# Kernel optimization log

Measured on AMD Instinct MI355X. Metric: run time of the kernel, lower is better.

## Reference

```python
import jax, jax.numpy as jnp
import numpy as np

NPG = 39      # nodes per graph, from (1+8+64+9)*(39+1)=3280 = lin1 in_features
NEG_SLOPE = 0.2


def gat_conv(x, src, dst, W, a_src, a_dst, b, n):
    """PyG GATConv, heads=1, self-loops already appended to (src, dst).
    x:[N,Fin] W:[Fin,Fout] a_src/a_dst:[Fout] b:[Fout] -> [N,Fout]"""
    h = x @ W                                        # [N,Fout]
    e = jax.nn.leaky_relu(h[src] @ a_src + h[dst] @ a_dst, NEG_SLOPE)  # [E]
    m = jax.lax.stop_gradient(jax.ops.segment_max(e, dst, num_segments=n))
    w = jnp.exp(e - m[dst])
    denom = jax.ops.segment_sum(w, dst, num_segments=n)
    alpha = w / (denom[dst] + 1e-16)                 # segment softmax per target node
    out = jax.ops.segment_sum(alpha[:, None] * h[src], dst, num_segments=n)
    return out + b


def setup_inputs() -> dict:
    key = jax.random.key(0)
    ks = jax.random.split(key, 20)
    B, DEG = 4096, 8
    N = B * NPG
    E = N * DEG
    x = jax.random.normal(ks[0], (N, 1), dtype=jnp.float32)
    # block-diagonal edges: each node emits DEG edges to random nodes in SAME graph
    src = jnp.repeat(jnp.arange(N, dtype=jnp.int64), DEG)
    offs = (src // NPG) * NPG
    dst = offs + jax.random.randint(ks[1], (E,), 0, NPG, dtype=jnp.int64)
    edge_index = jnp.stack([src, dst])
    batch_vec = jnp.repeat(jnp.arange(B, dtype=jnp.int64), NPG)

    def glorot(k, shape):
        fan = shape[0] + (shape[1] if len(shape) > 1 else 1)
        s = jnp.sqrt(6.0 / fan)
        return jax.random.uniform(k, shape, jnp.float32, -s, s)

    p = {
        'W1': glorot(ks[2], (1, 8)),   'a1s': glorot(ks[3], (8,)),  'a1d': glorot(ks[4], (8,)),  'b1': jnp.zeros((8,), jnp.float32),
        'W2': glorot(ks[5], (8, 64)),  'a2s': glorot(ks[6], (64,)), 'a2d': glorot(ks[7], (64,)), 'b2': jnp.zeros((64,), jnp.float32),
        'W3': glorot(ks[8], (64, 9)),  'a3s': glorot(ks[9], (9,)),  'a3d': glorot(ks[10], (9,)), 'b3': jnp.zeros((9,), jnp.float32),
        'lW1': glorot(ks[11], (3280, 5000)), 'lb1': jnp.zeros((5000,), jnp.float32),
        'lW2': glorot(ks[12], (5000, 1024)), 'lb2': jnp.zeros((1024,), jnp.float32),
        'lW3': glorot(ks[13], (1024, 9)),    'lb3': jnp.zeros((9,), jnp.float32),
    }
    return {'x': x, 'edge_index': edge_index, 'batch_vec': batch_vec, **p}


def reference(x, edge_index, batch_vec,
              W1, a1s, a1d, b1, W2, a2s, a2d, b2, W3, a3s, a3d, b3,
              lW1, lb1, lW2, lb2, lW3, lb3):
    N = x.shape[0]
    B = N // NPG
    loops = jnp.arange(N, dtype=edge_index.dtype)
    src = jnp.concatenate([edge_index[0], loops])   # GATConv add_self_loops=True
    dst = jnp.concatenate([edge_index[1], loops])

    res = x.reshape(B, -1)                                    # [B,39]
    out0 = jax.ops.segment_max(x, batch_vec, num_segments=B)  # [B,1]

    h1 = jax.nn.relu(gat_conv(x, src, dst, W1, a1s, a1d, b1, N))   # dropout = eval no-op
    res1 = h1.reshape(B, -1)                                   # [B,312]
    out1 = jax.ops.segment_max(h1, batch_vec, num_segments=B)

    h2 = jax.nn.relu(gat_conv(h1, src, dst, W2, a2s, a2d, b2, N))
    res2 = h2.reshape(B, -1)                                   # [B,2496]
    out2 = jax.ops.segment_max(h2, batch_vec, num_segments=B)

    h3 = jax.nn.relu(gat_conv(h2, src, dst, W3, a3s, a3d, b3, N))
    res3 = h3.reshape(B, -1)                                   # [B,351]
    out3 = jax.ops.segment_max(h3, batch_vec, num_segments=B)

    f = jnp.concatenate([res, res1, res2, res3, out0, out1, out2, out3], axis=1)  # [B,3280]
    f = jax.nn.relu(f @ lW1 + lb1)
    f = jax.nn.relu(f @ lW2 + lb2)
    return f @ lW3 + lb3                                       # [B,9]
```

## Files before the change

kernel.cpp:

```cpp
#include <hip/hip_runtime.h>
#include <hip/hip_bf16.h>
#include <hip/hip_fp16.h>
#include <stdint.h>


typedef float f32x4 __attribute__((ext_vector_type(4)));
typedef short bf16x8 __attribute__((ext_vector_type(8)));


__device__ __forceinline__ void seg_softmax(
    float* al, const unsigned short* sl, const int* off, float* sa,
    const float* dbuf, int L)
{
  if (L < 39) {
    int p0 = off[L], p1 = off[L + 1];
    float d = dbuf[L];
    float mx = -1e30f;
    for (int p = p0; p < p1; ++p) {
      float e = sa[sl[p]] + d;
      e = (e > 0.f) ? e : 0.2f * e;
      al[p] = e; mx = fmaxf(mx, e);
    }
    float den = 0.f;
    for (int p = p0; p < p1; ++p) { float wv = __expf(al[p] - mx); al[p] = wv; den += wv; }
    sa[L] = 1.f / (den + 1e-16f);
  }
}

__global__ __launch_bounds__(128) void gnn_block(
    const float* __restrict__ x,
    const int* __restrict__ esrc, const int* __restrict__ edst,
    const float* __restrict__ W1, const float* __restrict__ a1s, const float* __restrict__ a1d, const float* __restrict__ b1,
    const float* __restrict__ W2, const float* __restrict__ a2s, const float* __restrict__ a2d, const float* __restrict__ b2,
    const float* __restrict__ W3, const float* __restrict__ a3s, const float* __restrict__ a3d, const float* __restrict__ b3,
    __hip_bfloat16* __restrict__ fA)
{
  __shared__ __align__(16) char HtU[5152];
  __shared__ __align__(16) __half h2buf[2576];
  __shared__ float h3b[352];
  __shared__ __half h1h[320];
  __shared__ float al[352];
  __shared__ unsigned short sl[352];
  __shared__ int off[40];
  __shared__ int cur[40];
  __shared__ float sa[40], dbuf[40], xbuf[40];
  __shared__ float a2buf[128];
  __shared__ float mx[132];
  __shared__ float sW3s[576];

  const int tid = threadIdx.x, g = blockIdx.x;
  float* Hf  = (float*)HtU;
  __half* Hh = (__half*)HtU;

  const int rt = g >> 7, mi = (g >> 4) & 7, lrow = g & 15;
  const size_t gbase = (size_t)rt * 52 * 8192 + (size_t)(mi * 2) * 512 + (size_t)lrow * 8;
#define COLADDR(c) (gbase + (size_t)((c) >> 6) * 8192 + (size_t)(((c) >> 5) & 1) * 512 \
                    + (size_t)(((c) >> 3) & 3) * 128 + ((c) & 7))

  for (int i = tid; i < 576; i += 128) sW3s[i] = W3[i];
  a2buf[tid] = (tid < 64) ? a2s[tid] : a2d[tid - 64];
  float xv = 0.f;
  if (tid < 40) cur[tid] = 0;
  if (tid < 39) { xv = x[g * 39 + tid]; xbuf[tid] = xv; }

  if (tid < 64) {
    float m = (tid < 39) ? xv : -1e30f;
    for (int o = 32; o >= 1; o >>= 1) m = fmaxf(m, __shfl_xor(m, o, 64));
    if (tid == 0) mx[0] = m;
  }
  if (tid < 39) fA[COLADDR(tid)] = __float2bfloat16(xv);
  __syncthreads();

  int els[3], eld[3];
  const int eb = g * 312, nb0 = g * 39;
#pragma unroll
  for (int it = 0; it < 3; ++it) {
    int e = it * 128 + tid, ls = -1, ld = 0;
    if (e < 351) {
      if (e < 312) { ls = esrc[eb + e] - nb0; ld = edst[eb + e] - nb0; }
      else         { ls = e - 312; ld = ls; }
      atomicAdd(&cur[ld], 1);
    }
    els[it] = ls; eld[it] = ld;
  }
  __syncthreads();
  if (tid < 64) {
    int c = (tid < 39) ? cur[tid] : 0;
    int incl = c;
    for (int o = 1; o < 64; o <<= 1) { int t = __shfl_up(incl, o, 64); if (tid >= o) incl += t; }
    if (tid < 39) off[tid] = incl - c;
    if (tid == 38) off[39] = incl;
  }
  __syncthreads();
  if (tid < 39) cur[tid] = off[tid];
  __syncthreads();
#pragma unroll
  for (int it = 0; it < 3; ++it)
    if (els[it] >= 0) { int p = atomicAdd(&cur[eld[it]], 1); sl[p] = (unsigned short)els[it]; }
  __syncthreads();

  {
    const float w1r = W1[tid & 7];
#pragma unroll
    for (int it = 0; it < 3; ++it) {
      int slot = it * 128 + tid;
      if (slot < 312) { int i = slot >> 3, fi = slot & 7; Hf[i * 9 + fi] = xbuf[i] * w1r; }
    }
  }
  __syncthreads();
  {
    int node = tid & 63;
    if (node < 39) {
      const float* av = (tid < 64) ? a1s : a1d;
      float s = 0.f;
#pragma unroll
      for (int f = 0; f < 8; ++f) s += Hf[node * 9 + f] * av[f];
      if (tid < 64) sa[node] = s; else dbuf[node] = s;
    }
  }
  __syncthreads();
  if (tid < 64) seg_softmax(al, sl, off, sa, dbuf, tid);
  __syncthreads();
  {
    const float b1r = b1[tid & 7];
#pragma unroll
    for (int it = 0; it < 3; ++it) {
      int slot = it * 128 + tid;
      if (slot < 312) {
        int i = slot >> 3, fi = slot & 7;
        float acc = 0.f;
        int p1 = off[i + 1];
        for (int p = off[i]; p < p1; ++p) acc += al[p] * Hf[sl[p] * 9 + fi];
        float v = fmaxf(acc * sa[i] + b1r, 0.f);
        h1h[i * 8 + fi] = __float2half(v);
        int c = 39 + slot;
        fA[COLADDR(c)] = __float2bfloat16(v);
      }
    }
  }
  __syncthreads();

  {
    const int f = tid & 63;
    float w2k[8];
#pragma unroll
    for (int k = 0; k < 8; ++k) w2k[k] = W2[k * 64 + f];
    for (int it = 0; it < 20; ++it) {
      int i = it * 2 + (tid >> 6);
      if (i < 39) {
        float hv = 0.f;
#pragma unroll
        for (int k = 0; k < 8; ++k) hv += __half2float(h1h[i * 8 + k]) * w2k[k];
        Hh[i * 66 + f] = __float2half(hv);
      }
    }
  }
  __syncthreads();
  {
    int node = tid & 63;
    if (node < 39) {
      const float* ab = a2buf + (tid & 64);
      float s = 0.f;
      for (int f = 0; f < 64; ++f) s += __half2float(Hh[node * 66 + f]) * ab[f];
      if (tid < 64) sa[node] = s; else dbuf[node] = s;
    }
  }
  __syncthreads();
  if (tid < 64) seg_softmax(al, sl, off, sa, dbuf, tid);
  __syncthreads();
  {
    const int f = tid & 63;
    const float b2r = b2[f];
    for (int it = 0; it < 20; ++it) {
      int i = it * 2 + (tid >> 6);
      if (i < 39) {
        float acc = 0.f;
        int p1 = off[i + 1];
        for (int p = off[i]; p < p1; ++p) acc += al[p] * __half2float(Hh[sl[p] * 66 + f]);
        float v = fmaxf(acc * sa[i] + b2r, 0.f);
        h2buf[i * 66 + f] = __float2half(v);
        int c = 351 + i * 64 + f;
        fA[COLADDR(c)] = __float2bfloat16(v);
      }
    }
  }
  __syncthreads();

  {
#pragma unroll
    for (int it = 0; it < 3; ++it) {
      int slot = it * 128 + tid;
      if (slot < 351) {
        int i = slot / 9, f3 = slot - 9 * i;
        float acc = 0.f;
        for (int k = 0; k < 64; ++k) acc += __half2float(h2buf[i * 66 + k]) * sW3s[k * 9 + f3];
        Hf[i * 10 + f3] = acc;
      }
    }
  }
  __syncthreads();
  {
    int node = tid & 63;
    if (node < 39) {
      const float* av = (tid < 64) ? a3s : a3d;
      float s = 0.f;
#pragma unroll
      for (int f3 = 0; f3 < 9; ++f3) s += Hf[node * 10 + f3] * av[f3];
      if (tid < 64) sa[node] = s; else dbuf[node] = s;
    }
  }
  __syncthreads();
  if (tid < 64) seg_softmax(al, sl, off, sa, dbuf, tid);
  __syncthreads();
  {
#pragma unroll
    for (int it = 0; it < 3; ++it) {
      int slot = it * 128 + tid;
      if (slot < 351) {
        int i = slot / 9, f3 = slot - 9 * i;
        float acc = 0.f;
        int p1 = off[i + 1];
        for (int p = off[i]; p < p1; ++p) acc += al[p] * Hf[sl[p] * 10 + f3];
        float v = fmaxf(acc * sa[i] + b3[f3], 0.f);
        h3b[slot] = v;
        int c = 2847 + slot;
        fA[COLADDR(c)] = __float2bfloat16(v);
      }
    }
  }
  __syncthreads();

  if (tid >= 1 && tid < 9) {
    int f = tid - 1; float m = -1e30f;
    for (int i = 0; i < 39; ++i) m = fmaxf(m, __half2float(h1h[i * 8 + f]));
    mx[tid] = m;
  } else if (tid >= 9 && tid < 73) {
    int f = tid - 9; float m = -1e30f;
    for (int i = 0; i < 39; ++i) m = fmaxf(m, __half2float(h2buf[i * 66 + f]));
    mx[tid] = m;
  } else if (tid >= 73 && tid < 82) {
    int f = tid - 73; float m = -1e30f;
    for (int i = 0; i < 39; ++i) m = fmaxf(m, h3b[i * 9 + f]);
    mx[tid] = m;
  } else if (tid >= 82 && tid < 130) {
    mx[tid] = 0.f;
  }
  __syncthreads();
  if (tid < 130) {
    int c = 3198 + tid;
    fA[COLADDR(c)] = __float2bfloat16(mx[tid]);
  }
#undef COLADDR
}


__global__ __launch_bounds__(256) void conv_tiled(
    const float* __restrict__ W, short* __restrict__ WT,
    int K0, int N0, int KT)
{
  __shared__ float t[64][68];
  const int kb = blockIdx.x * 64, nb = blockIdx.y * 64;
  const int tid = threadIdx.x;
  const int tx = tid & 15, ty = tid >> 4;
#pragma unroll
  for (int r = 0; r < 4; ++r) {
    int k = kb + ty + r * 16, n = nb + tx * 4;
    float4 v = make_float4(0.f, 0.f, 0.f, 0.f);
    if (k < K0 && n < N0) v = *(const float4*)&W[(size_t)k * N0 + n];
    t[ty + r * 16][tx * 4 + 0] = v.x; t[ty + r * 16][tx * 4 + 1] = v.y;
    t[ty + r * 16][tx * 4 + 2] = v.z; t[ty + r * 16][tx * 4 + 3] = v.w;
  }
  __syncthreads();
  const int nl = tid >> 2, kc0 = tid & 3;
#pragma unroll
  for (int h = 0; h < 2; ++h) {
    int kc = kc0 + h * 4;
    int n = nb + nl, k = kb + kc * 8;
    union { bf16x8 v; __hip_bfloat16 b[8]; } z;
#pragma unroll
    for (int j = 0; j < 8; ++j) z.b[j] = __float2bfloat16(t[kc * 8 + j][nl]);
    int rt = n >> 7, mi = (n >> 4) & 7, lr = n & 15;
    int kt = k >> 6, kq = (k >> 5) & 1, lc = (k >> 3) & 3;
    size_t addr = ((((size_t)rt * KT) + kt) * 16 + mi * 2 + kq) * 512 + ((size_t)lr + 16 * lc) * 8;
    *(bf16x8*)&WT[addr] = z.v;
  }
}


__device__ __forceinline__ void gld_lds16(const void* gptr, void* l) {
  typedef const __attribute__((address_space(1))) unsigned int GU;
  typedef __attribute__((address_space(3))) unsigned int LU;
  __builtin_amdgcn_global_load_lds((GU*)gptr, (LU*)l, 16, 0, 0);
}

template<int MODE>
__global__ __launch_bounds__(256) void gemm_tiled(
    const short* __restrict__ A, const short* __restrict__ B,
    const float* __restrict__ bias, int Nreal,
    void* __restrict__ Cout, int Nn, int KT, int ktPerSplit, int outKT)
{
  __shared__ __align__(16) short lA[8192];
  __shared__ __align__(16) short lB[8192];
  const int tid = threadIdx.x;
  const int w = tid >> 6, L = tid & 63;
  const int lrow = L & 15, lch = L >> 4;
  const int mt = blockIdx.y, nt = blockIdx.x;
  const int mw = (w >> 1) * 4, nw = (w & 1) * 4;
  const int kt0 = blockIdx.z * ktPerSplit, kt1 = kt0 + ktPerSplit;

  const short* Ab = A + ((size_t)mt * KT) * 8192 + (size_t)L * 8;
  const short* Bb = B + ((size_t)nt * KT) * 8192 + (size_t)L * 8;

  f32x4 acc[4][4] = {};

  for (int kt = kt0; kt < kt1; ++kt) {
    const short* Ak = Ab + (size_t)kt * 8192;
    const short* Bk = Bb + (size_t)kt * 8192;
#pragma unroll
    for (int j = 0; j < 4; ++j) {
      int st = w * 4 + j;
      gld_lds16(Ak + st * 512, &lA[st * 512]);
      gld_lds16(Bk + st * 512, &lB[st * 512]);
    }
    __syncthreads();
#pragma unroll
    for (int kk = 0; kk < 2; ++kk) {
      bf16x8 af[4], bfr[4];
#pragma unroll
      for (int i = 0; i < 4; ++i) {
        af[i]  = *(const bf16x8*)&lA[((mw + i) * 2 + kk) * 512 + L * 8];
        bfr[i] = *(const bf16x8*)&lB[((nw + i) * 2 + kk) * 512 + L * 8];
      }
#pragma unroll
      for (int i = 0; i < 4; ++i)
#pragma unroll
        for (int j = 0; j < 4; ++j)
          acc[i][j] = __builtin_amdgcn_mfma_f32_16x16x32_bf16(af[i], bfr[j], acc[i][j], 0, 0, 0);
    }
    __syncthreads();
  }

  if (MODE == 0) {
    __hip_bfloat16* C = (__hip_bfloat16*)Cout;
#pragma unroll
    for (int j = 0; j < 4; ++j) {
      int n = nt * 128 + (nw + j) * 16 + lrow;
      float bn = (n < Nreal) ? bias[n] : 0.f;
      int kt = n >> 6, kq = (n >> 5) & 1, lc2 = (n >> 3) & 3, j2 = n & 7;
#pragma unroll
      for (int i = 0; i < 4; ++i) {
        int mi = mw + i;
        size_t base = ((((size_t)mt * outKT + kt) * 16) + mi * 2 + kq) * 512
                      + (size_t)(lch * 4) * 8 + (size_t)lc2 * 128 + j2;
#pragma unroll
        for (int r = 0; r < 4; ++r)
          C[base + r * 8] = __float2bfloat16(fmaxf(acc[i][j][r] + bn, 0.f));
      }
    }
  } else {
    float* P = (float*)Cout + (size_t)blockIdx.z * 4096 * 1024;
#pragma unroll
    for (int j = 0; j < 4; ++j) {
      int n = nt * 128 + (nw + j) * 16 + lrow;
#pragma unroll
      for (int i = 0; i < 4; ++i)
#pragma unroll
        for (int r = 0; r < 4; ++r) {
          int m = mt * 128 + (mw + i) * 16 + lch * 4 + r;
          P[(size_t)m * Nn + n] = acc[i][j][r];
        }
    }
  }
}


__global__ __launch_bounds__(256) void gemm3_fused(
    const float* __restrict__ P,
    const float* __restrict__ b2v,
    const float* __restrict__ W3,
    const float* __restrict__ b3v,
    float* __restrict__ out)
{
  __shared__ float sW3[9 * 1024];
  int tid = threadIdx.x;
  for (int i = tid; i < 9216; i += 256) { int k = i / 9, j = i - 9 * k; sW3[j * 1024 + k] = W3[i]; }
  __syncthreads();
  int row = blockIdx.x * 4 + (tid >> 6);
  int lane = tid & 63;
  const float* p0 = P + (size_t)row * 1024;
  const float* p1 = p0 + (size_t)4096 * 1024;
  float acc[9] = {0, 0, 0, 0, 0, 0, 0, 0, 0};
  for (int t = 0; t < 16; ++t) {
    int k = lane + 64 * t;
    float c = fmaxf(p0[k] + p1[k] + b2v[k], 0.f);
#pragma unroll
    for (int j = 0; j < 9; ++j) acc[j] += c * sW3[j * 1024 + k];
  }
#pragma unroll
  for (int j = 0; j < 9; ++j) {
    float v = acc[j];
    v += __shfl_down(v, 32, 64);
    v += __shfl_down(v, 16, 64);
    v += __shfl_down(v, 8, 64);
    v += __shfl_down(v, 4, 64);
    v += __shfl_down(v, 2, 64);
    v += __shfl_down(v, 1, 64);
    if (lane == 0) out[(size_t)row * 9 + j] = v + b3v[j];
  }
}


extern "C" void kernel_launch(void* const* d_in, const int* in_sizes, int n_in,
                              void* d_out, int out_size, void* d_ws, size_t ws_size,
                              hipStream_t stream)
{
  const float* x   = (const float*)d_in[0];
  const int*   ei  = (const int*)d_in[1];
  const float* W1  = (const float*)d_in[3];
  const float* a1s = (const float*)d_in[4];
  const float* a1d = (const float*)d_in[5];
  const float* b1  = (const float*)d_in[6];
  const float* W2  = (const float*)d_in[7];
  const float* a2s = (const float*)d_in[8];
  const float* a2d = (const float*)d_in[9];
  const float* b2  = (const float*)d_in[10];
  const float* W3  = (const float*)d_in[11];
  const float* a3s = (const float*)d_in[12];
  const float* a3d = (const float*)d_in[13];
  const float* b3  = (const float*)d_in[14];
  const float* lW1 = (const float*)d_in[15];
  const float* lb1 = (const float*)d_in[16];
  const float* lW2 = (const float*)d_in[17];
  const float* lb2 = (const float*)d_in[18];
  const float* lW3 = (const float*)d_in[19];
  const float* lb3 = (const float*)d_in[20];

  const int E = 4096 * 39 * 8;
  const int* esrc = ei;
  const int* edst = ei + E;

  short* fA  = (short*)d_ws;
  short* W1T = fA  + (size_t)4096 * 3328;
  short* C1  = W1T + (size_t)5120 * 3328;
  short* W2T = C1  + (size_t)4096 * 5120;
  float* P   = (float*)d_ws;

  conv_tiled<<<dim3(3328 / 64, 5120 / 64), 256, 0, stream>>>(lW1, W1T, 3280, 5000, 52);
  conv_tiled<<<dim3(5120 / 64, 1024 / 64), 256, 0, stream>>>(lW2, W2T, 5000, 1024, 80);
  gnn_block<<<4096, 128, 0, stream>>>(x, esrc, edst,
                                      W1, a1s, a1d, b1, W2, a2s, a2d, b2, W3, a3s, a3d, b3,
                                      (__hip_bfloat16*)fA);
  gemm_tiled<0><<<dim3(40, 32, 1), 256, 0, stream>>>(fA, W1T, lb1, 5000, C1, 5120, 52, 52, 80);
  gemm_tiled<1><<<dim3(8, 32, 2), 256, 0, stream>>>(C1, W2T, nullptr, 1024, P, 1024, 80, 40, 0);
  gemm3_fused<<<1024, 256, 0, stream>>>(P, lb2, lW3, lb3, (float*)d_out);
}
```

Measured before the change: 487.9 us.

## Replace CSR segment softmax with dense per-graph attention matrix and atomics

New measurement: 502.7 us. +3.0%, slower.

```diff
diff --git a/kernel.cpp b/kernel.cpp
--- a/kernel.cpp
+++ b/kernel.cpp
@@ -7,25 +7,15 @@
 typedef float f32x4 __attribute__((ext_vector_type(4)));
 typedef short bf16x8 __attribute__((ext_vector_type(8)));
 
-
-__device__ __forceinline__ void seg_softmax(
-    float* al, const unsigned short* sl, const int* off, float* sa,
-    const float* dbuf, int L)
-{
-  if (L < 39) {
-    int p0 = off[L], p1 = off[L + 1];
-    float d = dbuf[L];
-    float mx = -1e30f;
-    for (int p = p0; p < p1; ++p) {
-      float e = sa[sl[p]] + d;
-      e = (e > 0.f) ? e : 0.2f * e;
-      al[p] = e; mx = fmaxf(mx, e);
-    }
-    float den = 0.f;
-    for (int p = p0; p < p1; ++p) { float wv = __expf(al[p] - mx); al[p] = wv; den += wv; }
-    sa[L] = 1.f / (den + 1e-16f);
-  }
-}
+__device__ __forceinline__ unsigned fenc(float f) {
+  int s = __float_as_int(f);
+  return s < 0 ? ~(unsigned)s : ((unsigned)s | 0x80000000u);
+}
+__device__ __forceinline__ float fdec(unsigned u) {
+  return (u & 0x80000000u) ? __int_as_float((int)(u & 0x7fffffffu))
+                           : __int_as_float(~(int)u);
+}
+
 
 __global__ __launch_bounds__(128) void gnn_block(
     const float* __restrict__ x,
@@ -36,16 +26,14 @@
     __hip_bfloat16* __restrict__ fA)
 {
   __shared__ __align__(16) char HtU[5152];
-  __shared__ __align__(16) __half h2buf[2576];
-  __shared__ float h3b[352];
-  __shared__ __half h1h[320];
-  __shared__ float al[352];
-  __shared__ unsigned short sl[352];
-  __shared__ int off[40];
-  __shared__ int cur[40];
-  __shared__ float sa[40], dbuf[40], xbuf[40];
+  __shared__ __align__(16) __half h2buf[2574];
+  __shared__ __align__(16) __half h1h[312];
+  __shared__ float A[1599];
+  __shared__ float den[40];
+  __shared__ unsigned umax[40];
+  __shared__ float sarr[40], darr[40], xbuf[40];
   __shared__ float a2buf[128];
-  __shared__ float mx[132];
+  __shared__ unsigned umx[132];
   __shared__ float sW3s[576];
 
   const int tid = threadIdx.x, g = blockIdx.x;
@@ -59,17 +47,12 @@
 
   for (int i = tid; i < 576; i += 128) sW3s[i] = W3[i];
   a2buf[tid] = (tid < 64) ? a2s[tid] : a2d[tid - 64];
+  for (int i = tid; i < 132; i += 128) umx[i] = 0u;
+  for (int i = tid; i < 1599; i += 128) A[i] = 0.f;
+  if (tid < 39) { den[tid] = 0.f; umax[tid] = 0u; }
+
   float xv = 0.f;
-  if (tid < 40) cur[tid] = 0;
-  if (tid < 39) { xv = x[g * 39 + tid]; xbuf[tid] = xv; }
-
-  if (tid < 64) {
-    float m = (tid < 39) ? xv : -1e30f;
-    for (int o = 32; o >= 1; o >>= 1) m = fmaxf(m, __shfl_xor(m, o, 64));
-    if (tid == 0) mx[0] = m;
-  }
-  if (tid < 39) fA[COLADDR(tid)] = __float2bfloat16(xv);
-  __syncthreads();
+  if (tid < 39) { xv = x[g * 39 + tid]; xbuf[tid] = xv; fA[COLADDR(tid)] = __float2bfloat16(xv); }
 
   int els[3], eld[3];
   const int eb = g * 312, nb0 = g * 39;
@@ -79,74 +62,63 @@
     if (e < 351) {
       if (e < 312) { ls = esrc[eb + e] - nb0; ld = edst[eb + e] - nb0; }
       else         { ls = e - 312; ld = ls; }
-      atomicAdd(&cur[ld], 1);
     }
     els[it] = ls; eld[it] = ld;
   }
-  __syncthreads();
-  if (tid < 64) {
-    int c = (tid < 39) ? cur[tid] : 0;
-    int incl = c;
-    for (int o = 1; o < 64; o <<= 1) { int t = __shfl_up(incl, o, 64); if (tid >= o) incl += t; }
-    if (tid < 39) off[tid] = incl - c;
-    if (tid == 38) off[39] = incl;
-  }
-  __syncthreads();
-  if (tid < 39) cur[tid] = off[tid];
-  __syncthreads();
-#pragma unroll
-  for (int it = 0; it < 3; ++it)
-    if (els[it] >= 0) { int p = atomicAdd(&cur[eld[it]], 1); sl[p] = (unsigned short)els[it]; }
+  float c_s = 0.f, c_d = 0.f;
+  float w1r = W1[tid & 7], b1r = b1[tid & 7];
+#pragma unroll
+  for (int f = 0; f < 8; ++f) { float wv = W1[f]; c_s += wv * a1s[f]; c_d += wv * a1d[f]; }
+  __syncthreads();
+
+  if (tid < 39) atomicMax(&umx[0], fenc(xv));
+  float ee[3];
+#pragma unroll
+  for (int it = 0; it < 3; ++it) {
+    if (els[it] >= 0) {
+      float e = xbuf[els[it]] * c_s + xbuf[eld[it]] * c_d;
+      e = (e > 0.f) ? e : 0.2f * e;
+      ee[it] = e;
+      atomicMax(&umax[eld[it]], fenc(e));
+    }
+  }
+  __syncthreads();
+#pragma unroll
+  for (int it = 0; it < 3; ++it) {
+    if (els[it] >= 0) {
+      float wv = __expf(ee[it] - fdec(umax[eld[it]]));
+      atomicAdd(&den[eld[it]], wv);
+      atomicAdd(&A[eld[it] * 41 + els[it]], wv);
+    }
+  }
+  __syncthreads();
+  if (tid < 39) {
+    float q = 0.f;
+#pragma unroll
+    for (int k = 0; k < 39; ++k) q += A[tid * 41 + k] * xbuf[k];
+    sarr[tid] = q * (1.f / (den[tid] + 1e-16f));
+  }
+  __syncthreads();
+#pragma unroll
+  for (int it = 0; it < 3; ++it) {
+    int slot = it * 128 + tid;
+    if (slot < 312) {
+      int i = slot >> 3, fi = slot & 7;
+      float v = fmaxf(sarr[i] * w1r + b1r, 0.f);
+      h1h[slot] = __float2half(v);
+      fA[COLADDR(39 + slot)] = __float2bfloat16(v);
+      atomicMax(&umx[1 + fi], fenc(v));
+    }
+  }
   __syncthreads();
 
   {
-    const float w1r = W1[tid & 7];
-#pragma unroll
-    for (int it = 0; it < 3; ++it) {
-      int slot = it * 128 + tid;
-      if (slot < 312) { int i = slot >> 3, fi = slot & 7; Hf[i * 9 + fi] = xbuf[i] * w1r; }
-    }
-  }
-  __syncthreads();
-  {
-    int node = tid & 63;
-    if (node < 39) {
-      const float* av = (tid < 64) ? a1s : a1d;
-      float s = 0.f;
-#pragma unroll
-      for (int f = 0; f < 8; ++f) s += Hf[node * 9 + f] * av[f];
-      if (tid < 64) sa[node] = s; else dbuf[node] = s;
-    }
-  }
-  __syncthreads();
-  if (tid < 64) seg_softmax(al, sl, off, sa, dbuf, tid);
-  __syncthreads();
-  {
-    const float b1r = b1[tid & 7];
-#pragma unroll
-    for (int it = 0; it < 3; ++it) {
-      int slot = it * 128 + tid;
-      if (slot < 312) {
-        int i = slot >> 3, fi = slot & 7;
-        float acc = 0.f;
-        int p1 = off[i + 1];
-        for (int p = off[i]; p < p1; ++p) acc += al[p] * Hf[sl[p] * 9 + fi];
-        float v = fmaxf(acc * sa[i] + b1r, 0.f);
-        h1h[i * 8 + fi] = __float2half(v);
-        int c = 39 + slot;
-        fA[COLADDR(c)] = __float2bfloat16(v);
-      }
-    }
-  }
-  __syncthreads();
-
-  {
-    const int f = tid & 63;
+    const int f = tid & 63, wv2 = tid >> 6;
     float w2k[8];
 #pragma unroll
     for (int k = 0; k < 8; ++k) w2k[k] = W2[k * 64 + f];
     for (int it = 0; it < 20; ++it) {
-      int i = it * 2 + (tid >> 6);
+      int i = it * 2 + wv2;
       if (i < 39) {
         float hv = 0.f;
 #pragma unroll
@@ -154,33 +126,51 @@
         Hh[i * 66 + f] = __float2half(hv);
       }
     }
-  }
-  __syncthreads();
-  {
-    int node = tid & 63;
-    if (node < 39) {
-      const float* ab = a2buf + (tid & 64);
-      float s = 0.f;
-      for (int f = 0; f < 64; ++f) s += __half2float(Hh[node * 66 + f]) * ab[f];
-      if (tid < 64) sa[node] = s; else dbuf[node] = s;
-    }
-  }
-  __syncthreads();
-  if (tid < 64) seg_softmax(al, sl, off, sa, dbuf, tid);
-  __syncthreads();
-  {
-    const int f = tid & 63;
+    for (int i = tid; i < 1599; i += 128) A[i] = 0.f;
+    if (tid < 39) { den[tid] = 0.f; umax[tid] = 0u; }
+    __syncthreads();
+    {
+      int node = tid & 63;
+      if (node < 39) {
+        const float* ab = a2buf + (tid & 64);
+        float s = 0.f;
+#pragma unroll
+        for (int f2 = 0; f2 < 64; ++f2) s += __half2float(Hh[node * 66 + f2]) * ab[f2];
+        if (tid < 64) sarr[node] = s; else darr[node] = s;
+      }
+    }
+    __syncthreads();
+#pragma unroll
+    for (int it = 0; it < 3; ++it) {
+      if (els[it] >= 0) {
+        float e = sarr[els[it]] + darr[eld[it]];
+        e = (e > 0.f) ? e : 0.2f * e;
+        ee[it] = e;
+        atomicMax(&umax[eld[it]], fenc(e));
+      }
+    }
+    __syncthreads();
+#pragma unroll
+    for (int it = 0; it < 3; ++it) {
+      if (els[it] >= 0) {
+        float wv = __expf(ee[it] - fdec(umax[eld[it]]));
+        atomicAdd(&den[eld[it]], wv);
+        atomicAdd(&A[eld[it] * 41 + els[it]], wv);
+      }
+    }
+    __syncthreads();
     const float b2r = b2[f];
     for (int it = 0; it < 20; ++it) {
-      int i = it * 2 + (tid >> 6);
+      int i = it * 2 + wv2;
       if (i < 39) {
+        float inv = 1.f / (den[i] + 1e-16f);
         float acc = 0.f;
-        int p1 = off[i + 1];
-        for (int p = off[i]; p < p1; ++p) acc += al[p] * __half2float(Hh[sl[p] * 66 + f]);
-        float v = fmaxf(acc * sa[i] + b2r, 0.f);
+#pragma unroll
+        for (int k = 0; k < 39; ++k) acc += A[i * 41 + k] * __half2float(Hh[k * 66 + f]);
+        float v = fmaxf(acc * inv + b2r, 0.f);
         h2buf[i * 66 + f] = __float2half(v);
-        int c = 351 + i * 64 + f;
-        fA[COLADDR(c)] = __float2bfloat16(v);
+        fA[COLADDR(351 + i * 64 + f)] = __float2bfloat16(v);
+        atomicMax(&umx[9 + f], fenc(v));
       }
     }
   }
@@ -193,62 +183,65 @@
       if (slot < 351) {
         int i = slot / 9, f3 = slot - 9 * i;
         float acc = 0.f;
+#pragma unroll
         for (int k = 0; k < 64; ++k) acc += __half2float(h2buf[i * 66 + k]) * sW3s[k * 9 + f3];
         Hf[i * 10 + f3] = acc;
       }
     }
-  }
-  __syncthreads();
-  {
-    int node = tid & 63;
-    if (node < 39) {
-      const float* av = (tid < 64) ? a3s : a3d;
-      float s = 0.f;
-#pragma unroll
-      for (int f3 = 0; f3 < 9; ++f3) s += Hf[node * 10 + f3] * av[f3];
-      if (tid < 64) sa[node] = s; else dbuf[node] = s;
-    }
-  }
-  __syncthreads();
-  if (tid < 64) seg_softmax(al, sl, off, sa, dbuf, tid);
-  __syncthreads();
-  {
+    for (int i = tid; i < 1599; i += 128) A[i] = 0.f;
+    if (tid < 39) { den[tid] = 0.f; umax[tid] = 0u; }
+    __syncthreads();
+    {
+      int node = tid & 63;
+      if (node < 39) {
+        const float* av = (tid < 64) ? a3s : a3d;
+        float s = 0.f;
+#pragma unroll
+        for (int f3 = 0; f3 < 9; ++f3) s += Hf[node * 10 + f3] * av[f3];
+        if (tid < 64) sarr[node] = s; else darr[node] = s;
+      }
+    }
+    __syncthreads();
+#pragma unroll
+    for (int it = 0; it < 3; ++it) {
+      if (els[it] >= 0) {
+        float e = sarr[els[it]] + darr[eld[it]];
+        e = (e > 0.f) ? e : 0.2f * e;
+        ee[it] = e;
+        atomicMax(&umax[eld[it]], fenc(e));
+      }
+    }
+    __syncthreads();
+#pragma unroll
+    for (int it = 0; it < 3; ++it) {
+      if (els[it] >= 0) {
+        float wv = __expf(ee[it] - fdec(umax[eld[it]]));
+        atomicAdd(&den[eld[it]], wv);
+        atomicAdd(&A[eld[it] * 41 + els[it]], wv);
+      }
+    }
+    __syncthreads();
 #pragma unroll
     for (int it = 0; it < 3; ++it) {
       int slot = it * 128 + tid;
       if (slot < 351) {
         int i = slot / 9, f3 = slot - 9 * i;
+        float inv = 1.f / (den[i] + 1e-16f);
         float acc = 0.f;
-        int p1 = off[i + 1];
-        for (int p = off[i]; p < p1; ++p) acc += al[p] * Hf[sl[p] * 10 + f3];
-        float v = fmaxf(acc * sa[i] + b3[f3], 0.f);
-        h3b[slot] = v;
-        int c = 2847 + slot;
-        fA[COLADDR(c)] = __float2bfloat16(v);
-      }
-    }
-  }
-  __syncthreads();
-
-  if (tid >= 1 && tid < 9) {
-    int f = tid - 1; float m = -1e30f;
-    for (int i = 0; i < 39; ++i) m = fmaxf(m, __half2float(h1h[i * 8 + f]));
-    mx[tid] = m;
-  } else if (tid >= 9 && tid < 73) {
-    int f = tid - 9; float m = -1e30f;
-    for (int i = 0; i < 39; ++i) m = fmaxf(m, __half2float(h2buf[i * 66 + f]));
-    mx[tid] = m;
-  } else if (tid >= 73 && tid < 82) {
-    int f = tid - 73; float m = -1e30f;
-    for (int i = 0; i < 39; ++i) m = fmaxf(m, h3b[i * 9 + f]);
-    mx[tid] = m;
-  } else if (tid >= 82 && tid < 130) {
-    mx[tid] = 0.f;
-  }
-  __syncthreads();
+#pragma unroll
+        for (int k = 0; k < 39; ++k) acc += A[i * 41 + k] * Hf[k * 10 + f3];
+        float v = fmaxf(acc * inv + b3[f3], 0.f);
+        fA[COLADDR(2847 + slot)] = __float2bfloat16(v);
+        atomicMax(&umx[73 + f3], fenc(v));
+      }
+    }
+  }
+  __syncthreads();
+
   if (tid < 130) {
     int c = 3198 + tid;
-    fA[COLADDR(c)] = __float2bfloat16(mx[tid]);
+    float v = (tid < 82) ? fdec(umx[tid]) : 0.f;
+    fA[COLADDR(c)] = __float2bfloat16(v);
   }
 #undef COLADDR
 }
```
